# Performance work log

Hardware: AMD Instinct MI355X
Metric: run time of the kernel (lower is better)

Reference implementation:

```python
import jax, jax.numpy as jnp
import numpy as np

N, E = 50000, 800000
IN, HID, OUT = 256, 128, 128


def setup_inputs() -> dict:
    key = jax.random.key(0)
    ks = jax.random.split(key, 6)
    x = jax.random.normal(ks[0], (N, IN), dtype=jnp.float32)
    edge_index = jax.random.randint(ks[1], (2, E), 0, N, dtype=jnp.int32)
    # xavier_normal-ish scales (exact init values irrelevant for correctness baseline)
    W1 = jax.random.normal(ks[2], (IN, HID), dtype=jnp.float32) * (1.414 / np.sqrt(IN))
    att_src = jax.random.normal(ks[3], (HID,), dtype=jnp.float32) * 0.1
    att_dst = jax.random.normal(ks[4], (HID,), dtype=jnp.float32) * 0.1
    W2 = jax.random.normal(ks[5], (HID, OUT), dtype=jnp.float32) * (1.414 / np.sqrt(HID))
    return {"x": x, "edge_index": edge_index, "W1": W1,
            "att_src": att_src, "att_dst": att_dst, "W2": W2}


def _gat_layer(x, edge_index, W, a_src, a_dst):
    """GATConv(heads=1, concat=False, add_self_loops=False, dropout=0), attention=True."""
    n = x.shape[0]
    src, dst = edge_index[0], edge_index[1]  # message x_j = h[src], grouped by index = dst
    h = x @ W                                 # (N, C)
    e_src = h @ a_src                         # (N,) per-node attention logits
    e_dst = h @ a_dst                         # (N,)
    # per-edge: sigmoid(alpha_j + alpha_i), then scatter-softmax over dst neighborhoods
    alpha = jax.nn.sigmoid(e_src[src] + e_dst[dst])             # (E,)
    m = jax.ops.segment_max(alpha, dst, num_segments=n)          # stable softmax max
    ex = jnp.exp(alpha - m[dst])
    denom = jax.ops.segment_sum(ex, dst, num_segments=n)
    w = ex / denom[dst]                                          # (E,)
    # scatter-add aggregation of weighted source features; heads=1 so mean over heads is identity
    return jax.ops.segment_sum(h[src] * w[:, None], dst, num_segments=n)  # (N, C)


def reference(x, edge_index, W1, att_src, att_dst, W2):
    h1 = jax.nn.elu(_gat_layer(x, edge_index, W1, att_src, att_dst))
    # conv2 called with attention=False: mm(h1, W2).view(N,1,C).mean(1) == plain linear
    return h1 @ W2
```

## Files before the change

### kernel.cpp

```cpp
#include <hip/hip_runtime.h>
#include <hip/hip_bf16.h>

#define N_NODES 50000
#define N_EDGES 800000
#define DIN 256
#define DHID 128
#define DOUT 128
#define NBUCK 196
#define BINBLK 256
#define EPB 3125
#define BINIT 13

typedef __attribute__((ext_vector_type(8))) short bf16x8;
typedef __attribute__((ext_vector_type(4))) float f32x4;

__device__ inline unsigned short f2b(float f) {
    __hip_bfloat16 b = __float2bfloat16(f);
    return *reinterpret_cast<unsigned short*>(&b);
}

__global__ __launch_bounds__(256) void convW_kernel(
    const float* __restrict__ W1, const float* __restrict__ W2,
    unsigned short* __restrict__ W1t, unsigned short* __restrict__ W2t)
{
    int i = blockIdx.x * 256 + threadIdx.x;
    if (i < DIN * DHID) {
        int n = i >> 8, k = i & 255;
        W1t[i] = f2b(W1[k * DHID + n]);
    } else {
        int j = i - DIN * DHID;
        int n = j >> 7, k = j & 127;
        W2t[j] = f2b(W2[k * DOUT + n]);
    }
}

__global__ __launch_bounds__(256) void gemm1_mfma(
    const float* __restrict__ x,
    const unsigned short* __restrict__ W1t,
    const float* __restrict__ att_src,
    const float* __restrict__ att_dst,
    unsigned short* __restrict__ hb,
    float* __restrict__ es,
    float* __restrict__ ed)
{
    __shared__ unsigned short W1s[DHID * DIN];

    const int tid = threadIdx.x;
    const int wave = tid >> 6, lane = tid & 63;
    const int row0 = blockIdx.x * 64 + wave * 16;
    const int m = lane & 15, q = lane >> 4;

    {
        const float4* src = (const float4*)W1t;
        float4* dst = (float4*)W1s;
        #pragma unroll
        for (int i = 0; i < 16; ++i)
            dst[tid + i * 256] = src[tid + i * 256];
    }
    __syncthreads();

    int r  = row0 + m;
    int rc = (r < N_NODES) ? r : 0;

    f32x4 acc[8];
    #pragma unroll
    for (int t = 0; t < 8; ++t) acc[t] = (f32x4){0.f, 0.f, 0.f, 0.f};

    const float* xr = x + (size_t)rc * DIN + q * 8;
    const short* wp = (const short*)W1s + q * 8;

    #pragma unroll
    for (int kt = 0; kt < 8; ++kt) {
        float4 f0 = *(const float4*)(xr + kt * 32);
        float4 f1 = *(const float4*)(xr + kt * 32 + 4);
        bf16x8 a;
        a[0] = (short)f2b(f0.x); a[1] = (short)f2b(f0.y);
        a[2] = (short)f2b(f0.z); a[3] = (short)f2b(f0.w);
        a[4] = (short)f2b(f1.x); a[5] = (short)f2b(f1.y);
        a[6] = (short)f2b(f1.z); a[7] = (short)f2b(f1.w);
        #pragma unroll
        for (int t = 0; t < 8; ++t) {
            bf16x8 b = *(const bf16x8*)(wp + (t * 16 + m) * DIN + kt * 32);
            acc[t] = __builtin_amdgcn_mfma_f32_16x16x32_bf16(a, b, acc[t], 0, 0, 0);
        }
    }

    #pragma unroll
    for (int reg = 0; reg < 4; ++reg) {
        int rr = row0 + q * 4 + reg;
        if (rr < N_NODES) {
            #pragma unroll
            for (int t = 0; t < 8; ++t)
                hb[(size_t)rr * DHID + t * 16 + m] = f2b(acc[t][reg]);
        }
    }

    float esr[4] = {0.f, 0.f, 0.f, 0.f}, edr[4] = {0.f, 0.f, 0.f, 0.f};
    #pragma unroll
    for (int t = 0; t < 8; ++t) {
        float as = att_src[t * 16 + m];
        float ad = att_dst[t * 16 + m];
        #pragma unroll
        for (int reg = 0; reg < 4; ++reg) {
            esr[reg] += acc[t][reg] * as;
            edr[reg] += acc[t][reg] * ad;
        }
    }
    #pragma unroll
    for (int off = 8; off; off >>= 1)
        #pragma unroll
        for (int reg = 0; reg < 4; ++reg) {
            esr[reg] += __shfl_xor(esr[reg], off);
            edr[reg] += __shfl_xor(edr[reg], off);
        }
    if (m == 0) {
        #pragma unroll
        for (int reg = 0; reg < 4; ++reg) {
            int rr = row0 + q * 4 + reg;
            if (rr < N_NODES) { es[rr] = esr[reg]; ed[rr] = edr[reg]; }
        }
    }
}

__global__ __launch_bounds__(256) void lhist_kernel(
    const int* __restrict__ ei, int* __restrict__ blockHist,
    int* __restrict__ bucketTotals)
{
    __shared__ int h[NBUCK];
    const int t = threadIdx.x, blk = blockIdx.x;
    if (t < NBUCK) h[t] = 0;
    __syncthreads();
    const int base = blk * EPB;
    #pragma unroll 1
    for (int it = 0; it < BINIT; ++it) {
        int e = base + it * 256 + t;
        if (e < base + EPB)
            atomicAdd(&h[ei[N_EDGES + e] >> 8], 1);
    }
    __syncthreads();
    if (t < NBUCK) {
        blockHist[t * 256 + blk] = h[t];
        atomicAdd(&bucketTotals[t], h[t]);
    }
}

__global__ __launch_bounds__(256) void scanfused_kernel(
    const int* __restrict__ bucketTotals,
    const int* __restrict__ blockHist,
    int* __restrict__ matrixScan)
{
    __shared__ int bs[256];
    __shared__ int s[256];
    const int t = threadIdx.x, b = blockIdx.x;

    bs[t] = (t < NBUCK) ? bucketTotals[t] : 0;
    __syncthreads();
    #pragma unroll
    for (int off = 1; off < 256; off <<= 1) {
        int u = (t >= off) ? bs[t - off] : 0;
        __syncthreads();
        bs[t] += u;
        __syncthreads();
    }
    const int base = (b == 0) ? 0 : bs[b - 1];

    int c = blockHist[b * 256 + t];
    s[t] = c;
    __syncthreads();
    #pragma unroll
    for (int off = 1; off < 256; off <<= 1) {
        int u = (t >= off) ? s[t - off] : 0;
        __syncthreads();
        s[t] += u;
        __syncthreads();
    }
    matrixScan[b * 256 + t] = base + s[t] - c;
}

__global__ __launch_bounds__(256) void binpass_kernel(
    const int* __restrict__ ei,
    const float* __restrict__ es,
    const float* __restrict__ ed,
    const int* __restrict__ matrixScan,
    int2* __restrict__ binned)
{
    __shared__ int lcur[NBUCK];
    const int t = threadIdx.x, blk = blockIdx.x;
    if (t < NBUCK) lcur[t] = matrixScan[t * 256 + blk];
    __syncthreads();
    const int base = blk * EPB;
    #pragma unroll 1
    for (int it = 0; it < BINIT; ++it) {
        int e = base + it * 256 + t;
        if (e < base + EPB) {
            int s = ei[e];
            int d = ei[N_EDGES + e];
            float a  = es[s] + ed[d];
            float sg = 1.f / (1.f + __expf(-a));
            float w  = __expf(sg);
            int pos = atomicAdd(&lcur[d >> 8], 1);
            binned[pos] = make_int2(s | ((d & 255) << 16), __float_as_int(w));
        }
    }
}

__global__ __launch_bounds__(256) void sortpass_kernel(
    const int2* __restrict__ binned,
    const int* __restrict__ matrixScan,
    int2* __restrict__ sortedSW,
    int* __restrict__ offset,
    int* __restrict__ count)
{
    __shared__ int lhist[256], lscan[256], lcur[256];
    const int t = threadIdx.x, b = blockIdx.x;
    const int start = matrixScan[b * 256];
    const int end   = (b == NBUCK - 1) ? N_EDGES : matrixScan[(b + 1) * 256];
    const int cnt   = end - start;

    lhist[t] = 0;
    __syncthreads();
    for (int i = t; i < cnt; i += 256)
        atomicAdd(&lhist[(binned[start + i].x >> 16) & 255], 1);
    __syncthreads();

    int v = lhist[t];
    lscan[t] = v;
    __syncthreads();
    #pragma unroll
    for (int off = 1; off < 256; off <<= 1) {
        int u = (t >= off) ? lscan[t - off] : 0;
        __syncthreads();
        lscan[t] += u;
        __syncthreads();
    }
    int excl = lscan[t] - v;

    int node = (b << 8) + t;
    if (node < N_NODES) { offset[node] = start + excl; count[node] = v; }
    lcur[t] = excl;
    __syncthreads();

    for (int i = t; i < cnt; i += 256) {
        int2 ent = binned[start + i];
        int dlow = (ent.x >> 16) & 255;
        int pos = atomicAdd(&lcur[dlow], 1);
        sortedSW[start + pos] = make_int2(ent.x & 0xFFFF, ent.y);
    }
}

__global__ __launch_bounds__(256) void agg_kernel(
    const int2* __restrict__ sortedSW,
    const int* __restrict__ offset,
    const int* __restrict__ count,
    const unsigned short* __restrict__ hb,
    unsigned int* __restrict__ h1b)
{
    int node = (blockIdx.x * 256 + threadIdx.x) >> 6;
    int lane = threadIdx.x & 63;
    if (node >= N_NODES) return;

    int beg = offset[node];
    int deg = count[node];

    float2 acc = make_float2(0.f, 0.f);
    float wsum = 0.f;

    for (int base = 0; base < deg; base += 64) {
        int cnt = min(64, deg - base);
        int2 sw = (lane < cnt) ? sortedSW[beg + base + lane] : make_int2(0, 0);
        int j = 0;

#define TIER(T)                                                                 \
        for (; j + T <= cnt; j += T) {                                          \
            unsigned uu[T]; float ww[T];                                        \
            _Pragma("unroll")                                                   \
            for (int k = 0; k < T; ++k) {                                       \
                int s_ = __builtin_amdgcn_readlane(sw.x, j + k);                \
                uu[k] = *(const unsigned*)(hb + (size_t)s_ * DHID + 2 * lane);  \
            }                                                                   \
            _Pragma("unroll")                                                   \
            for (int k = 0; k < T; ++k)                                         \
                ww[k] = __uint_as_float(                                        \
                    (unsigned)__builtin_amdgcn_readlane(sw.y, j + k));          \
            _Pragma("unroll")                                                   \
            for (int k = 0; k < T; ++k) {                                       \
                wsum  += ww[k];                                                 \
                acc.x += ww[k] * __uint_as_float(uu[k] << 16);                  \
                acc.y += ww[k] * __uint_as_float(uu[k] & 0xffff0000u);          \
            }                                                                   \
        }

        TIER(16)
        TIER(8)
        TIER(4)
#undef TIER
        for (; j < cnt; ++j) {
            int   sj = __builtin_amdgcn_readlane(sw.x, j);
            float wj = __uint_as_float((unsigned)__builtin_amdgcn_readlane(sw.y, j));
            unsigned u = *(const unsigned*)(hb + (size_t)sj * DHID + 2 * lane);
            acc.x += wj * __uint_as_float(u << 16);
            acc.y += wj * __uint_as_float(u & 0xffff0000u);
            wsum  += wj;
        }
    }
    float inv = (deg > 0) ? 1.f / wsum : 0.f;
    float v0 = acc.x * inv, v1 = acc.y * inv;
    float e0 = v0 > 0.f ? v0 : (__expf(v0) - 1.f);
    float e1 = v1 > 0.f ? v1 : (__expf(v1) - 1.f);
    h1b[(size_t)node * (DHID / 2) + lane] =
        (unsigned)f2b(e0) | ((unsigned)f2b(e1) << 16);
}

__global__ __launch_bounds__(256) void gemm2_mfma(
    const unsigned short* __restrict__ h1b,
    const unsigned short* __restrict__ W2t,
    float* __restrict__ out)
{
    __shared__ unsigned short W2s[DOUT * DHID];

    const int tid = threadIdx.x;
    const int wave = tid >> 6, lane = tid & 63;
    const int row0 = blockIdx.x * 64 + wave * 16;
    const int m = lane & 15, q = lane >> 4;

    {
        const float4* src = (const float4*)W2t;
        float4* dst = (float4*)W2s;
        #pragma unroll
        for (int i = 0; i < 8; ++i)
            dst[tid + i * 256] = src[tid + i * 256];
    }
    __syncthreads();

    int r  = row0 + m;
    int rc = (r < N_NODES) ? r : 0;

    f32x4 acc[8];
    #pragma unroll
    for (int t = 0; t < 8; ++t) acc[t] = (f32x4){0.f, 0.f, 0.f, 0.f};

    const short* xp = (const short*)h1b + (size_t)rc * DHID + q * 8;
    const short* wp = (const short*)W2s + q * 8;

    #pragma unroll
    for (int kt = 0; kt < 4; ++kt) {
        bf16x8 a = *(const bf16x8*)(xp + kt * 32);
        #pragma unroll
        for (int t = 0; t < 8; ++t) {
            bf16x8 b = *(const bf16x8*)(wp + (t * 16 + m) * DHID + kt * 32);
            acc[t] = __builtin_amdgcn_mfma_f32_16x16x32_bf16(a, b, acc[t], 0, 0, 0);
        }
    }

    #pragma unroll
    for (int reg = 0; reg < 4; ++reg) {
        int rr = row0 + q * 4 + reg;
        if (rr < N_NODES) {
            #pragma unroll
            for (int t = 0; t < 8; ++t)
                out[(size_t)rr * DOUT + t * 16 + m] = acc[t][reg];
        }
    }
}

extern "C" void kernel_launch(void* const* d_in, const int* in_sizes, int n_in,
                              void* d_out, int out_size, void* d_ws, size_t ws_size,
                              hipStream_t stream)
{
    const float* x    = (const float*)d_in[0];
    const int*   ei   = (const int*)d_in[1];
    const float* W1   = (const float*)d_in[2];
    const float* asrc = (const float*)d_in[3];
    const float* adst = (const float*)d_in[4];
    const float* W2   = (const float*)d_in[5];
    float*       out  = (float*)d_out;

    char* p = (char*)d_ws;
    unsigned short* hb  = (unsigned short*)p;  p += (size_t)N_NODES * DHID * 2;
    unsigned int*   h1b = (unsigned int*)p;    p += (size_t)N_NODES * DHID * 2;
    unsigned short* W1t = (unsigned short*)p;  p += (size_t)DHID * DIN * 2;
    unsigned short* W2t = (unsigned short*)p;  p += (size_t)DOUT * DHID * 2;
    float* es     = (float*)p;  p += (size_t)N_NODES * 4;
    float* ed     = (float*)p;  p += (size_t)N_NODES * 4;
    int*   offset = (int*)p;    p += (size_t)N_NODES * 4;
    int*   count  = (int*)p;    p += (size_t)N_NODES * 4;
    int*   blockHist    = (int*)p; p += (size_t)NBUCK * 256 * 4;
    int*   matrixScan   = (int*)p; p += (size_t)NBUCK * 256 * 4;
    int*   bucketTotals = (int*)p; p += 256 * 4;
    int2*  binned   = (int2*)p; p += (size_t)N_EDGES * 8;
    int2*  sortedSW = (int2*)p; p += (size_t)N_EDGES * 8;

    hipMemsetAsync(bucketTotals, 0, NBUCK * sizeof(int), stream);

    convW_kernel<<<(DIN * DHID + DHID * DOUT) / 256, 256, 0, stream>>>(W1, W2, W1t, W2t);

    gemm1_mfma<<<(N_NODES + 63) / 64, 256, 0, stream>>>(x, W1t, asrc, adst, hb, es, ed);

    lhist_kernel    <<<BINBLK, 256, 0, stream>>>(ei, blockHist, bucketTotals);
    scanfused_kernel<<<NBUCK, 256, 0, stream>>>(bucketTotals, blockHist, matrixScan);
    binpass_kernel  <<<BINBLK, 256, 0, stream>>>(ei, es, ed, matrixScan, binned);
    sortpass_kernel <<<NBUCK, 256, 0, stream>>>(binned, matrixScan, sortedSW, offset, count);

    agg_kernel<<<(N_NODES * 64 + 255) / 256, 256, 0, stream>>>(
        sortedSW, offset, count, hb, h1b);

    gemm2_mfma<<<(N_NODES + 63) / 64, 256, 0, stream>>>((const unsigned short*)h1b, W2t, out);
}
```

Measured before the change: 198.1 us.

## Fuse weight conversion with histogram and scan with gemm1, pre-swizzle weight fragments

Merges weight conversion and the per-block edge histogram into one launch, and runs the bucket scan as extra blocks of the gemm1 launch. This drops two kernel launches and a memset, and removes the global bucketTotals atomics because each scan block recomputes the totals from blockHist. Weights are now stored in MFMA fragment order, so each lane loads contiguous 16-byte B fragments from LDS instead of strided rows, which should reduce LDS bank conflicts. In exchange, every scan block redundantly sums the whole histogram.

```diff
diff --git a/kernel.cpp b/kernel.cpp
--- a/kernel.cpp
+++ b/kernel.cpp
@@ -10,6 +10,7 @@
 #define BINBLK 256
 #define EPB 3125
 #define BINIT 13
+#define G1BLK ((N_NODES + 63) / 64)
 
 typedef __attribute__((ext_vector_type(8))) short bf16x8;
 typedef __attribute__((ext_vector_type(4))) float f32x4;
@@ -19,33 +20,98 @@
     return *reinterpret_cast<unsigned short*>(&b);
 }
 
-__global__ __launch_bounds__(256) void convW_kernel(
+__global__ __launch_bounds__(256) void convW_lhist_kernel(
     const float* __restrict__ W1, const float* __restrict__ W2,
-    unsigned short* __restrict__ W1t, unsigned short* __restrict__ W2t)
-{
-    int i = blockIdx.x * 256 + threadIdx.x;
-    if (i < DIN * DHID) {
-        int n = i >> 8, k = i & 255;
-        W1t[i] = f2b(W1[k * DHID + n]);
-    } else {
-        int j = i - DIN * DHID;
-        int n = j >> 7, k = j & 127;
-        W2t[j] = f2b(W2[k * DOUT + n]);
-    }
-}
-
-__global__ __launch_bounds__(256) void gemm1_mfma(
+    const int* __restrict__ ei,
+    unsigned short* __restrict__ W1t, unsigned short* __restrict__ W2t,
+    int* __restrict__ blockHist)
+{
+    __shared__ int h[NBUCK];
+    const int blk = blockIdx.x;
+    const int tid = threadIdx.x;
+
+    if (blk < 192) {
+        int i = blk * 256 + tid;
+        if (i < DIN * DHID) {
+            int n = i >> 8, k = i & 255;
+            int kt = k >> 5, q = (k >> 3) & 3, e = k & 7;
+            int t = n >> 4, m = n & 15;
+            W1t[(((kt * 8 + t) * 64) + (q * 16 + m)) * 8 + e] = f2b(W1[k * DHID + n]);
+        } else {
+            int j = i - DIN * DHID;
+            int n = j >> 7, k = j & 127;
+            int kt = k >> 5, q = (k >> 3) & 3, e = k & 7;
+            int t = n >> 4, m = n & 15;
+            W2t[(((kt * 8 + t) * 64) + (q * 16 + m)) * 8 + e] = f2b(W2[k * DOUT + n]);
+        }
+        return;
+    }
+
+    const int b = blk - 192;
+    if (tid < NBUCK) h[tid] = 0;
+    __syncthreads();
+    const int base = b * EPB;
+    #pragma unroll 1
+    for (int it = 0; it < BINIT; ++it) {
+        int e = base + it * 256 + tid;
+        if (e < base + EPB)
+            atomicAdd(&h[ei[N_EDGES + e] >> 8], 1);
+    }
+    __syncthreads();
+    if (tid < NBUCK) blockHist[tid * 256 + b] = h[tid];
+}
+
+__global__ __launch_bounds__(256) void gemm1_scan_kernel(
     const float* __restrict__ x,
     const unsigned short* __restrict__ W1t,
     const float* __restrict__ att_src,
     const float* __restrict__ att_dst,
+    const int* __restrict__ blockHist,
     unsigned short* __restrict__ hb,
     float* __restrict__ es,
-    float* __restrict__ ed)
+    float* __restrict__ ed,
+    int* __restrict__ matrixScan)
 {
     __shared__ unsigned short W1s[DHID * DIN];
 
     const int tid = threadIdx.x;
+
+    if (blockIdx.x >= G1BLK) {
+        int* bs = (int*)W1s;
+        int* s  = bs + 256;
+        const int b = blockIdx.x - G1BLK;
+
+        int tot = 0;
+        if (tid < NBUCK) {
+            const int* row = blockHist + tid * 256;
+            #pragma unroll 4
+            for (int i = 0; i < 256; ++i) tot += row[i];
+        }
+        bs[tid] = tot;
+        __syncthreads();
+        #pragma unroll
+        for (int off = 1; off < 256; off <<= 1) {
+            int u = (tid >= off) ? bs[tid - off] : 0;
+            __syncthreads();
+            bs[tid] += u;
+            __syncthreads();
+        }
+        const int base = (b == 0) ? 0 : bs[b - 1];
+
+        int c = blockHist[b * 256 + tid];
+        s[tid] = c;
+        __syncthreads();
+        #pragma unroll
+        for (int off = 1; off < 256; off <<= 1) {
+            int u = (tid >= off) ? s[tid - off] : 0;
+            __syncthreads();
+            s[tid] += u;
+            __syncthreads();
+        }
+        matrixScan[b * 256 + tid] = base + s[tid] - c;
+        return;
+    }
+
     const int wave = tid >> 6, lane = tid & 63;
     const int row0 = blockIdx.x * 64 + wave * 16;
     const int m = lane & 15, q = lane >> 4;
@@ -67,7 +133,7 @@
     for (int t = 0; t < 8; ++t) acc[t] = (f32x4){0.f, 0.f, 0.f, 0.f};
 
     const float* xr = x + (size_t)rc * DIN + q * 8;
-    const short* wp = (const short*)W1s + q * 8;
+    const short* wfrag = (const short*)W1s + lane * 8;
 
     #pragma unroll
     for (int kt = 0; kt < 8; ++kt) {
@@ -80,7 +146,7 @@
         a[6] = (short)f2b(f1.z); a[7] = (short)f2b(f1.w);
         #pragma unroll
         for (int t = 0; t < 8; ++t) {
-            bf16x8 b = *(const bf16x8*)(wp + (t * 16 + m) * DIN + kt * 32);
+            bf16x8 b = *(const bf16x8*)(wfrag + (kt * 8 + t) * 512);
             acc[t] = __builtin_amdgcn_mfma_f32_16x16x32_bf16(a, b, acc[t], 0, 0, 0);
         }
     }
@@ -120,61 +186,6 @@
             if (rr < N_NODES) { es[rr] = esr[reg]; ed[rr] = edr[reg]; }
         }
     }
-}
-
-__global__ __launch_bounds__(256) void lhist_kernel(
-    const int* __restrict__ ei, int* __restrict__ blockHist,
-    int* __restrict__ bucketTotals)
-{
-    __shared__ int h[NBUCK];
-    const int t = threadIdx.x, blk = blockIdx.x;
-    if (t < NBUCK) h[t] = 0;
-    __syncthreads();
-    const int base = blk * EPB;
-    #pragma unroll 1
-    for (int it = 0; it < BINIT; ++it) {
-        int e = base + it * 256 + t;
-        if (e < base + EPB)
-            atomicAdd(&h[ei[N_EDGES + e] >> 8], 1);
-    }
-    __syncthreads();
-    if (t < NBUCK) {
-        blockHist[t * 256 + blk] = h[t];
-        atomicAdd(&bucketTotals[t], h[t]);
-    }
-}
-
-__global__ __launch_bounds__(256) void scanfused_kernel(
-    const int* __restrict__ bucketTotals,
-    const int* __restrict__ blockHist,
-    int* __restrict__ matrixScan)
-{
-    __shared__ int bs[256];
-    __shared__ int s[256];
-    const int t = threadIdx.x, b = blockIdx.x;
-
-    bs[t] = (t < NBUCK) ? bucketTotals[t] : 0;
-    __syncthreads();
-    #pragma unroll
-    for (int off = 1; off < 256; off <<= 1) {
-        int u = (t >= off) ? bs[t - off] : 0;
-        __syncthreads();
-        bs[t] += u;
-        __syncthreads();
-    }
-    const int base = (b == 0) ? 0 : bs[b - 1];
-
-    int c = blockHist[b * 256 + t];
-    s[t] = c;
-    __syncthreads();
-    #pragma unroll
-    for (int off = 1; off < 256; off <<= 1) {
-        int u = (t >= off) ? s[t - off] : 0;
-        __syncthreads();
-        s[t] += u;
-        __syncthreads();
-    }
-    matrixScan[b * 256 + t] = base + s[t] - c;
 }
 
 __global__ __launch_bounds__(256) void binpass_kernel(
@@ -340,14 +351,14 @@
     for (int t = 0; t < 8; ++t) acc[t] = (f32x4){0.f, 0.f, 0.f, 0.f};
 
     const short* xp = (const short*)h1b + (size_t)rc * DHID + q * 8;
-    const short* wp = (const short*)W2s + q * 8;
+    const short* wfrag = (const short*)W2s + lane * 8;
 
     #pragma unroll
     for (int kt = 0; kt < 4; ++kt) {
         bf16x8 a = *(const bf16x8*)(xp + kt * 32);
         #pragma unroll
         for (int t = 0; t < 8; ++t) {
-            bf16x8 b = *(const bf16x8*)(wp + (t * 16 + m) * DHID + kt * 32);
+            bf16x8 b = *(const bf16x8*)(wfrag + (kt * 8 + t) * 512);
             acc[t] = __builtin_amdgcn_mfma_f32_16x16x32_bf16(a, b, acc[t], 0, 0, 0);
         }
     }
@@ -386,23 +397,17 @@
     int*   count  = (int*)p;    p += (size_t)N_NODES * 4;
     int*   blockHist    = (int*)p; p += (size_t)NBUCK * 256 * 4;
     int*   matrixScan   = (int*)p; p += (size_t)NBUCK * 256 * 4;
-    int*   bucketTotals = (int*)p; p += 256 * 4;
     int2*  binned   = (int2*)p; p += (size_t)N_EDGES * 8;
     int2*  sortedSW = (int2*)p; p += (size_t)N_EDGES * 8;
 
-    hipMemsetAsync(bucketTotals, 0, NBUCK * sizeof(int), stream);
-
-    convW_kernel<<<(DIN * DHID + DHID * DOUT) / 256, 256, 0, stream>>>(W1, W2, W1t, W2t);
-
-    gemm1_mfma<<<(N_NODES + 63) / 64, 256, 0, stream>>>(x, W1t, asrc, adst, hb, es, ed);
-
-    lhist_kernel    <<<BINBLK, 256, 0, stream>>>(ei, blockHist, bucketTotals);
-    scanfused_kernel<<<NBUCK, 256, 0, stream>>>(bucketTotals, blockHist, matrixScan);
+    convW_lhist_kernel<<<192 + BINBLK, 256, 0, stream>>>(W1, W2, ei, W1t, W2t, blockHist);
+
+    gemm1_scan_kernel<<<G1BLK + NBUCK, 256, 0, stream>>>(
+        x, W1t, asrc, adst, blockHist, hb, es, ed, matrixScan);
+
     binpass_kernel  <<<BINBLK, 256, 0, stream>>>(ei, es, ed, matrixScan, binned);
     sortpass_kernel <<<NBUCK, 256, 0, stream>>>(binned, matrixScan, sortedSW, offset, count);
-
     agg_kernel<<<(N_NODES * 64 + 255) / 256, 256, 0, stream>>>(
         sortedSW, offset, count, hb, h1b);
-
-    gemm2_mfma<<<(N_NODES + 63) / 64, 256, 0, stream>>>((const unsigned short*)h1b, W2t, out);
-}
+    gemm2_mfma<<<G1BLK, 256, 0, stream>>>((const unsigned short*)h1b, W2t, out);
+}
```

Result: faster. 187.3 us (-5.5%).
